# Kernel tuning notes

Hardware: AMD Instinct MI355X
Metric: run time of the kernel (lower is better)

Reference implementation:

```python
import jax, jax.numpy as jnp
import numpy as np

N_NODES = 50000
N_EDGES = 600000
N_GRAPHS = 256
D = 128
D_OUT = 32
NEG_SLOPE = 0.01
EPS = 1e-12


def setup_inputs() -> dict:
    key = jax.random.key(0)
    ks = jax.random.split(key, 10)
    x = jax.random.normal(ks[0], (N_NODES, D), dtype=jnp.float32)
    edge_index = jax.random.randint(ks[1], (2, N_EDGES), 0, N_NODES, dtype=jnp.int64)
    batch = jnp.sort(jax.random.randint(ks[2], (N_NODES,), 0, N_GRAPHS, dtype=jnp.int64))
    s = 1.0 / np.sqrt(D)
    return {
        "x": x,
        "edge_index": edge_index,
        "batch": batch,
        "W_fc1": jax.random.normal(ks[3], (D, D), dtype=jnp.float32) * s,
        "b_fc1": jnp.zeros((D,), dtype=jnp.float32),
        "W_gc1": jax.random.normal(ks[4], (D, D), dtype=jnp.float32) * s,
        "b_gc1": jnp.zeros((D,), dtype=jnp.float32),
        "W_gc2": jax.random.normal(ks[5], (D, D), dtype=jnp.float32) * s,
        "b_gc2": jnp.zeros((D,), dtype=jnp.float32),
        "W_fc2": jax.random.normal(ks[6], (D, D), dtype=jnp.float32) * s,
        "b_fc2": jnp.zeros((D,), dtype=jnp.float32),
        "W_fc3": jax.random.normal(ks[7], (D, D_OUT), dtype=jnp.float32) * s,
        "b_fc3": jnp.zeros((D_OUT,), dtype=jnp.float32),
    }


def _gcn_conv(h, src, dst, inv_sqrt_deg, inv_deg, W, b, n_nodes):
    # GCNConv with self-loops: out = D^{-1/2} (A+I) D^{-1/2} (h @ W) + b
    ht = h @ W  # [N, D]
    coef = inv_sqrt_deg[src] * inv_sqrt_deg[dst]  # [E]
    agg = jax.ops.segment_sum(ht[src] * coef[:, None], dst, num_segments=n_nodes)
    agg = agg + ht * inv_deg[:, None]  # self-loop term
    return agg + b


def reference(x, edge_index, batch, W_fc1, b_fc1, W_gc1, b_gc1, W_gc2, b_gc2,
              W_fc2, b_fc2, W_fc3, b_fc3):
    n = x.shape[0]
    src, dst = edge_index[0], edge_index[1]
    # degree with self-loops (in-degree over targets, unit edge weights)
    deg = jax.ops.segment_sum(jnp.ones_like(dst, dtype=x.dtype), dst, num_segments=n) + 1.0
    inv_sqrt_deg = jax.lax.rsqrt(deg)
    inv_deg = 1.0 / deg

    hx = x @ W_fc1 + b_fc1
    hx = jax.nn.leaky_relu(_gcn_conv(hx, src, dst, inv_sqrt_deg, inv_deg, W_gc1, b_gc1, n), NEG_SLOPE)
    hx = jax.nn.leaky_relu(_gcn_conv(hx, src, dst, inv_sqrt_deg, inv_deg, W_gc2, b_gc2, n), NEG_SLOPE)

    # global mean pool over graphs
    sums = jax.ops.segment_sum(hx, batch, num_segments=N_GRAPHS)  # [G, D]
    counts = jax.ops.segment_sum(jnp.ones((n,), dtype=x.dtype), batch, num_segments=N_GRAPHS)
    pooled = sums / jnp.maximum(counts, 1.0)[:, None]

    # L2 normalize (torch.nn.functional.normalize, p=2, dim=1)
    norm = jnp.sqrt(jnp.sum(pooled * pooled, axis=1, keepdims=True))
    hg = pooled / jnp.maximum(norm, EPS)

    h = jax.nn.leaky_relu(hg @ W_fc2 + b_fc2, NEG_SLOPE)
    out = h @ W_fc3 + b_fc3  # [G, D_OUT]
    return out
```

## Files before the change

kernel.cpp:

```cpp
#include <hip/hip_runtime.h>

#define N_NODES  50000
#define N_EDGES  600000
#define N_GRAPHS 256
#define DOUT     32
#define NEG      0.01f
#define SLOTS    64

typedef __attribute__((ext_vector_type(8))) short short8;
typedef __attribute__((ext_vector_type(4))) float f32x4;

__device__ __forceinline__ unsigned short bf16_rne(float x) {
    unsigned int u = __float_as_uint(x);
    return (unsigned short)((u + 0x7FFFu + ((u >> 16) & 1u)) >> 16);
}


__global__ __launch_bounds__(256) void k_pre(const float* __restrict__ W1,
                                             const float* __restrict__ b1,
                                             const float* __restrict__ W2,
                                             float* __restrict__ W12,
                                             float* __restrict__ b12,
                                             int* __restrict__ counts,
                                             const int* __restrict__ batch,
                                             int* __restrict__ gs,
                                             int* __restrict__ ge) {
    int bid = blockIdx.x;
    int tid = threadIdx.x;
    if (bid < 65) {
        int i = bid * 2 + (tid >> 7);
        int j = tid & 127;
        if (i < 129) {
            const float* left = (i < 128) ? (W1 + i * 128) : b1;
            float acc = 0.f;
#pragma unroll 4
            for (int k = 0; k < 128; ++k) acc += left[k] * W2[k * 128 + j];
            if (i < 128) W12[i * 128 + j] = acc;
            else b12[j] = acc;
        }
    } else if (bid < 261) {
        int i = (bid - 65) * 256 + tid;
        if (i < N_NODES) counts[i] = 0;
    } else {
        int i = (bid - 261) * 256 + tid;
        if (i < N_NODES) {
            int b = batch[i];
            if (i == 0 || batch[i - 1] != b) gs[b] = i;
            if (i == N_NODES - 1 || batch[i + 1] != b) ge[b] = i + 1;
        }
    }
}


__global__ __launch_bounds__(256) void k_degfill(const int* __restrict__ src,
                                                 const int* __restrict__ dst,
                                                 int* __restrict__ counts,
                                                 int* __restrict__ csrs) {
    int e = blockIdx.x * 256 + threadIdx.x;
    if (e < N_EDGES) {
        int s = src[e], d = dst[e];
        int slot = atomicAdd(&counts[d], 1);
        if (slot < SLOTS) csrs[(d << 6) + slot] = s;
    }
}


__global__ __launch_bounds__(256) void k_isd_gemm(
    const int* __restrict__ counts, float* __restrict__ isd,
    const float* __restrict__ Xf, const float* __restrict__ Wsrc,
    const float* __restrict__ bias, unsigned short* __restrict__ Y, int n)
{
    __shared__ short Wl[16384];
    int tid = threadIdx.x;
    int bid = blockIdx.x;
    if (bid < 196) {
        int i = bid * 256 + tid;
        if (i < N_NODES) isd[i] = rsqrtf((float)counts[i] + 1.0f);
        return;
    }
    bid -= 196;

    for (int idx = tid; idx < 16384; idx += 256) {
        float w = Wsrc[idx];
        int k = idx >> 7, c = idx & 127;
        int kt = k >> 5, nt = c >> 4;
        int lane = ((k & 31) >> 3) * 16 + (c & 15);
        int e = k & 7;
        Wl[((kt * 8 + nt) * 64 + lane) * 8 + e] = (short)bf16_rne(w);
    }
    __syncthreads();

    int wid = tid >> 6;
    int lane = tid & 63;
    int r0 = bid * 128 + wid * 32;
    int a0 = r0 + (lane & 15);      if (a0 >= n) a0 = n - 1;
    int a1 = r0 + 16 + (lane & 15); if (a1 >= n) a1 = n - 1;
    int ko = (lane >> 4) * 8;

    f32x4 acc0[8], acc1[8];
    f32x4 zero = {0.f, 0.f, 0.f, 0.f};
#pragma unroll
    for (int t = 0; t < 8; ++t) { acc0[t] = zero; acc1[t] = zero; }

#pragma unroll
    for (int kt = 0; kt < 4; ++kt) {
        int k0 = kt * 32 + ko;
        const float* p0 = Xf + (size_t)a0 * 128 + k0;
        const float* p1 = Xf + (size_t)a1 * 128 + k0;
        float4 u0 = *(const float4*)p0, u1 = *(const float4*)(p0 + 4);
        float4 v0 = *(const float4*)p1, v1 = *(const float4*)(p1 + 4);
        float us[8] = {u0.x, u0.y, u0.z, u0.w, u1.x, u1.y, u1.z, u1.w};
        float vs[8] = {v0.x, v0.y, v0.z, v0.w, v1.x, v1.y, v1.z, v1.w};
        short8 af0, af1;
#pragma unroll
        for (int i = 0; i < 8; ++i) {
            af0[i] = (short)bf16_rne(us[i]);
            af1[i] = (short)bf16_rne(vs[i]);
        }
#pragma unroll
        for (int t = 0; t < 8; ++t) {
            short8 bh = *(const short8*)&Wl[((kt * 8 + t) * 64 + lane) * 8];
            acc0[t] = __builtin_amdgcn_mfma_f32_16x16x32_bf16(af0, bh, acc0[t], 0, 0, 0);
            acc1[t] = __builtin_amdgcn_mfma_f32_16x16x32_bf16(af1, bh, acc1[t], 0, 0, 0);
        }
    }

    int rbase = r0 + (lane >> 4) * 4;
    int col0 = lane & 15;
#pragma unroll
    for (int t = 0; t < 8; ++t) {
        int col = t * 16 + col0;
        float badd = bias[col];
#pragma unroll
        for (int r = 0; r < 4; ++r) {
            int row0 = rbase + r;
            int row1 = rbase + 16 + r;
            if (row0 < n) Y[(size_t)row0 * 128 + col] = bf16_rne(acc0[t][r] + badd);
            if (row1 < n) Y[(size_t)row1 * 128 + col] = bf16_rne(acc1[t][r] + badd);
        }
    }
}


__global__ __launch_bounds__(256) void k_gemm_mfma(
    const unsigned short* __restrict__ Xh, const float* __restrict__ Wsrc,
    unsigned short* __restrict__ Y, int n)
{
    __shared__ short Wl[16384];
    int tid = threadIdx.x;
    for (int idx = tid; idx < 16384; idx += 256) {
        float w = Wsrc[idx];
        int k = idx >> 7, c = idx & 127;
        int kt = k >> 5, nt = c >> 4;
        int lane = ((k & 31) >> 3) * 16 + (c & 15);
        int e = k & 7;
        Wl[((kt * 8 + nt) * 64 + lane) * 8 + e] = (short)bf16_rne(w);
    }
    __syncthreads();

    int wid = tid >> 6;
    int lane = tid & 63;
    int r0 = blockIdx.x * 128 + wid * 32;
    int a0 = r0 + (lane & 15);      if (a0 >= n) a0 = n - 1;
    int a1 = r0 + 16 + (lane & 15); if (a1 >= n) a1 = n - 1;
    int ko = (lane >> 4) * 8;

    f32x4 acc0[8], acc1[8];
    f32x4 zero = {0.f, 0.f, 0.f, 0.f};
#pragma unroll
    for (int t = 0; t < 8; ++t) { acc0[t] = zero; acc1[t] = zero; }

#pragma unroll
    for (int kt = 0; kt < 4; ++kt) {
        int k0 = kt * 32 + ko;
        short8 af0 = *(const short8*)(Xh + (size_t)a0 * 128 + k0);
        short8 af1 = *(const short8*)(Xh + (size_t)a1 * 128 + k0);
#pragma unroll
        for (int t = 0; t < 8; ++t) {
            short8 bh = *(const short8*)&Wl[((kt * 8 + t) * 64 + lane) * 8];
            acc0[t] = __builtin_amdgcn_mfma_f32_16x16x32_bf16(af0, bh, acc0[t], 0, 0, 0);
            acc1[t] = __builtin_amdgcn_mfma_f32_16x16x32_bf16(af1, bh, acc1[t], 0, 0, 0);
        }
    }

    int rbase = r0 + (lane >> 4) * 4;
    int col0 = lane & 15;
#pragma unroll
    for (int t = 0; t < 8; ++t) {
        int col = t * 16 + col0;
#pragma unroll
        for (int r = 0; r < 4; ++r) {
            int row0 = rbase + r;
            int row1 = rbase + 16 + r;
            if (row0 < n) Y[(size_t)row0 * 128 + col] = bf16_rne(acc0[t][r]);
            if (row1 < n) Y[(size_t)row1 * 128 + col] = bf16_rne(acc1[t][r]);
        }
    }
}


__global__ __launch_bounds__(256) void k_agg(const unsigned short* __restrict__ HT,
                                             const int* __restrict__ csrs,
                                             const int* __restrict__ counts,
                                             const float* __restrict__ isd,
                                             const float* __restrict__ bias,
                                             unsigned short* __restrict__ OUT, int n) {
    int node = blockIdx.x * 4 + (threadIdx.x >> 6);
    int lane = threadIdx.x & 63;
    if (node >= n) return;
    const unsigned int* H = (const unsigned int*)HT;
    int base = node << 6;
    int cnt = counts[node]; cnt = cnt < SLOTS ? cnt : SLOTS;

    float is = isd[node];
    unsigned int su = H[(size_t)node * 64 + lane];
    float2 b = ((const float2*)bias)[lane];

    float acc0 = 0.f, acc1 = 0.f, acc2 = 0.f, acc3 = 0.f;
    int j = 0;
    for (; j + 8 <= cnt; j += 8) {
        int sx[8];
#pragma unroll
        for (int q = 0; q < 8; ++q) sx[q] = csrs[base + j + q];
        float cf[8];
#pragma unroll
        for (int q = 0; q < 8; ++q) cf[q] = isd[sx[q]];
        unsigned int v[8];
#pragma unroll
        for (int q = 0; q < 8; ++q) v[q] = H[(size_t)sx[q] * 64 + lane];
#pragma unroll
        for (int q = 0; q < 8; ++q) {
            float c = cf[q] * is;
            float f0 = __uint_as_float(v[q] << 16);
            float f1 = __uint_as_float(v[q] & 0xFFFF0000u);
            if (q & 1) { acc2 += f0 * c; acc3 += f1 * c; }
            else       { acc0 += f0 * c; acc1 += f1 * c; }
        }
    }
    for (; j + 4 <= cnt; j += 4) {
        int sx[4];
#pragma unroll
        for (int q = 0; q < 4; ++q) sx[q] = csrs[base + j + q];
        float cf[4];
#pragma unroll
        for (int q = 0; q < 4; ++q) cf[q] = isd[sx[q]];
        unsigned int v[4];
#pragma unroll
        for (int q = 0; q < 4; ++q) v[q] = H[(size_t)sx[q] * 64 + lane];
#pragma unroll
        for (int q = 0; q < 4; ++q) {
            float c = cf[q] * is;
            float f0 = __uint_as_float(v[q] << 16);
            float f1 = __uint_as_float(v[q] & 0xFFFF0000u);
            if (q & 1) { acc2 += f0 * c; acc3 += f1 * c; }
            else       { acc0 += f0 * c; acc1 += f1 * c; }
        }
    }
    for (; j < cnt; ++j) {
        int s = csrs[base + j];
        float c = isd[s] * is;
        unsigned int v = H[(size_t)s * 64 + lane];
        acc0 += __uint_as_float(v << 16) * c;
        acc1 += __uint_as_float(v & 0xFFFF0000u) * c;
    }

    float invd = is * is;
    float sv0 = __uint_as_float(su << 16);
    float sv1 = __uint_as_float(su & 0xFFFF0000u);
    float ox = acc0 + acc2 + sv0 * invd + b.x;
    float oy = acc1 + acc3 + sv1 * invd + b.y;
    ox = ox > 0.f ? ox : ox * NEG;
    oy = oy > 0.f ? oy : oy * NEG;
    unsigned int pk = (unsigned int)bf16_rne(ox) | ((unsigned int)bf16_rne(oy) << 16);
    ((unsigned int*)OUT)[(size_t)node * 64 + lane] = pk;
}


__global__ __launch_bounds__(256) void k_pool_final(const unsigned short* __restrict__ Hn,
                                                    const int* __restrict__ gs,
                                                    const int* __restrict__ ge,
                                                    const float* __restrict__ W2,
                                                    const float* __restrict__ b2,
                                                    const float* __restrict__ W3,
                                                    const float* __restrict__ b3,
                                                    float* __restrict__ out) {
    __shared__ float part[4][128];
    __shared__ float red[128];
    __shared__ float h1[128];
    int g = blockIdx.x, tid = threadIdx.x;
    int c2 = tid & 63, rr = tid >> 6;
    int s = gs[g], e = ge[g];
    const unsigned int* H = (const unsigned int*)Hn;
    float2 acc = make_float2(0.f, 0.f);
    for (int r = s + rr; r < e; r += 4) {
        unsigned int v = H[(size_t)r * 64 + c2];
        acc.x += __uint_as_float(v << 16);
        acc.y += __uint_as_float(v & 0xFFFF0000u);
    }
    part[rr][c2 * 2] = acc.x;
    part[rr][c2 * 2 + 1] = acc.y;
    __syncthreads();
    float mean = 0.f;
    if (tid < 128) {
        mean = (part[0][tid] + part[1][tid] + part[2][tid] + part[3][tid])
               / fmaxf((float)(e - s), 1.f);
        red[tid] = mean * mean;
    }
    __syncthreads();
    for (int off = 64; off > 0; off >>= 1) {
        if (tid < off) red[tid] += red[tid + off];
        __syncthreads();
    }
    if (tid < 128) {
        float norm = sqrtf(red[0]);
        part[0][tid] = mean / fmaxf(norm, 1e-12f);
    }
    __syncthreads();
    if (tid < 128) {
        float a = b2[tid];
#pragma unroll 8
        for (int k = 0; k < 128; ++k) a += part[0][k] * W2[k * 128 + tid];
        a = a > 0.f ? a : a * NEG;
        h1[tid] = a;
    }
    __syncthreads();
    if (tid < DOUT) {
        float a2 = b3[tid];
#pragma unroll 8
        for (int k = 0; k < 128; ++k) a2 += h1[k] * W3[k * DOUT + tid];
        out[g * DOUT + tid] = a2;
    }
}


extern "C" void kernel_launch(void* const* d_in, const int* in_sizes, int n_in,
                              void* d_out, int out_size, void* d_ws, size_t ws_size,
                              hipStream_t stream) {
    const float* x      = (const float*)d_in[0];
    const int*   ei     = (const int*)d_in[1];
    const int*   batch  = (const int*)d_in[2];
    const float* W_fc1  = (const float*)d_in[3];
    const float* b_fc1  = (const float*)d_in[4];
    const float* W_gc1  = (const float*)d_in[5];
    const float* b_gc1  = (const float*)d_in[6];
    const float* W_gc2  = (const float*)d_in[7];
    const float* b_gc2  = (const float*)d_in[8];
    const float* W_fc2  = (const float*)d_in[9];
    const float* b_fc2  = (const float*)d_in[10];
    const float* W_fc3  = (const float*)d_in[11];
    const float* b_fc3  = (const float*)d_in[12];
    float* out = (float*)d_out;

    const int N = N_NODES, E = N_EDGES;
    const int* e_src = ei;
    const int* e_dst = ei + E;

    char* ws = (char*)d_ws;
    unsigned short* H0     = (unsigned short*)(ws + 0);
    unsigned short* H1     = (unsigned short*)(ws + 12800000);
    float*          isd    = (float*)(ws + 25600000);
    int*            csrs   = (int*)  (ws + 25800000);
    int*            counts = (int*)  (ws + 38600000);
    int*            gs     = (int*)  (ws + 38800000);
    int*            ge     = (int*)  (ws + 38801024);
    float*          W12    = (float*)(ws + 38802048);
    float*          b12    = (float*)(ws + 38867584);

    const int EB = (E + 255) / 256;
    const int GB = (N + 127) / 128;

    k_pre<<<457, 256, 0, stream>>>(W_fc1, b_fc1, W_gc1, W12, b12, counts, batch, gs, ge);
    k_degfill<<<EB, 256, 0, stream>>>(e_src, e_dst, counts, csrs);
    k_isd_gemm<<<196 + GB, 256, 0, stream>>>(counts, isd, x, W12, b12, H1, N);
    k_agg<<<(N + 3) / 4, 256, 0, stream>>>(H1, csrs, counts, isd, b_gc1, H0, N);
    k_gemm_mfma<<<GB, 256, 0, stream>>>(H0, W_gc2, H1, N);
    k_agg<<<(N + 3) / 4, 256, 0, stream>>>(H1, csrs, counts, isd, b_gc2, H0, N);
    k_pool_final<<<N_GRAPHS, 256, 0, stream>>>(H0, gs, ge, W_fc2, b_fc2, W_fc3, b_fc3, out);

    (void)in_sizes; (void)n_in; (void)out_size; (void)ws_size;
}
```

Before: 162.0 us.

## Fuse edge fill into first GEMM and split CSR into primary/overflow slots

The degree/CSR fill is merged into the first GEMM launch as extra blocks, so both run concurrently and one launch is removed. The separate inverse-sqrt-degree array is dropped and recomputed with rsqrtf from the counts inside the aggregation kernel. Neighbor lists move to a compact 16-slot primary array plus a 48-slot overflow array, which shrinks the footprint the aggregation reads for typical degrees. In exchange, the fill blocks compete with the GEMM blocks for the GPU, and aggregation does an extra rsqrt per edge and takes a less unrolled path for high-degree nodes.

```diff
diff --git a/kernel.cpp b/kernel.cpp
--- a/kernel.cpp
+++ b/kernel.cpp
@@ -6,6 +6,9 @@
 #define DOUT     32
 #define NEG      0.01f
 #define SLOTS    64
+#define PSLOTS   16
+#define OSLOTS   48
+#define GB_GEMM  391
 
 typedef __attribute__((ext_vector_type(8))) short short8;
 typedef __attribute__((ext_vector_type(4))) float f32x4;
@@ -52,33 +55,26 @@
 }
 
 
-__global__ __launch_bounds__(256) void k_degfill(const int* __restrict__ src,
-                                                 const int* __restrict__ dst,
-                                                 int* __restrict__ counts,
-                                                 int* __restrict__ csrs) {
-    int e = blockIdx.x * 256 + threadIdx.x;
-    if (e < N_EDGES) {
-        int s = src[e], d = dst[e];
-        int slot = atomicAdd(&counts[d], 1);
-        if (slot < SLOTS) csrs[(d << 6) + slot] = s;
-    }
-}
-
-
-__global__ __launch_bounds__(256) void k_isd_gemm(
-    const int* __restrict__ counts, float* __restrict__ isd,
+__global__ __launch_bounds__(256) void k_fill_gemm(
+    const int* __restrict__ src, const int* __restrict__ dst,
+    int* __restrict__ counts, int* __restrict__ csrp, int* __restrict__ csro,
     const float* __restrict__ Xf, const float* __restrict__ Wsrc,
     const float* __restrict__ bias, unsigned short* __restrict__ Y, int n)
 {
     __shared__ short Wl[16384];
+    int bid = blockIdx.x;
     int tid = threadIdx.x;
-    int bid = blockIdx.x;
-    if (bid < 196) {
-        int i = bid * 256 + tid;
-        if (i < N_NODES) isd[i] = rsqrtf((float)counts[i] + 1.0f);
+
+    if (bid >= GB_GEMM) {
+        int e = (bid - GB_GEMM) * 256 + tid;
+        if (e < N_EDGES) {
+            int s = src[e], d = dst[e];
+            int slot = atomicAdd(&counts[d], 1);
+            if (slot < PSLOTS) csrp[(d << 4) + slot] = s;
+            else if (slot < SLOTS) csro[d * OSLOTS + slot - PSLOTS] = s;
+        }
         return;
     }
-    bid -= 196;
 
     for (int idx = tid; idx < 16384; idx += 256) {
         float w = Wsrc[idx];
@@ -200,65 +196,74 @@
 
 
 __global__ __launch_bounds__(256) void k_agg(const unsigned short* __restrict__ HT,
-                                             const int* __restrict__ csrs,
+                                             const int* __restrict__ csrp,
+                                             const int* __restrict__ csro,
                                              const int* __restrict__ counts,
-                                             const float* __restrict__ isd,
                                              const float* __restrict__ bias,
                                              unsigned short* __restrict__ OUT, int n) {
     int node = blockIdx.x * 4 + (threadIdx.x >> 6);
     int lane = threadIdx.x & 63;
     if (node >= n) return;
     const unsigned int* H = (const unsigned int*)HT;
-    int base = node << 6;
-    int cnt = counts[node]; cnt = cnt < SLOTS ? cnt : SLOTS;
-
-    float is = isd[node];
+    int deg = counts[node];
+    float is = rsqrtf((float)deg + 1.0f);
+    int c1 = deg < PSLOTS ? deg : PSLOTS;
+    int base = node << 4;
+
     unsigned int su = H[(size_t)node * 64 + lane];
     float2 b = ((const float2*)bias)[lane];
 
     float acc0 = 0.f, acc1 = 0.f, acc2 = 0.f, acc3 = 0.f;
     int j = 0;
-    for (; j + 8 <= cnt; j += 8) {
+    for (; j + 8 <= c1; j += 8) {
         int sx[8];
 #pragma unroll
-        for (int q = 0; q < 8; ++q) sx[q] = csrs[base + j + q];
-        float cf[8];
-#pragma unroll
-        for (int q = 0; q < 8; ++q) cf[q] = isd[sx[q]];
+        for (int q = 0; q < 8; ++q) sx[q] = csrp[base + j + q];
+        int dg[8];
+#pragma unroll
+        for (int q = 0; q < 8; ++q) dg[q] = counts[sx[q]];
         unsigned int v[8];
 #pragma unroll
         for (int q = 0; q < 8; ++q) v[q] = H[(size_t)sx[q] * 64 + lane];
 #pragma unroll
         for (int q = 0; q < 8; ++q) {
-            float c = cf[q] * is;
+            float c = rsqrtf((float)dg[q] + 1.0f) * is;
             float f0 = __uint_as_float(v[q] << 16);
             float f1 = __uint_as_float(v[q] & 0xFFFF0000u);
             if (q & 1) { acc2 += f0 * c; acc3 += f1 * c; }
             else       { acc0 += f0 * c; acc1 += f1 * c; }
         }
     }
-    for (; j + 4 <= cnt; j += 4) {
+    for (; j + 4 <= c1; j += 4) {
         int sx[4];
 #pragma unroll
-        for (int q = 0; q < 4; ++q) sx[q] = csrs[base + j + q];
-        float cf[4];
-#pragma unroll
-        for (int q = 0; q < 4; ++q) cf[q] = isd[sx[q]];
+        for (int q = 0; q < 4; ++q) sx[q] = csrp[base + j + q];
+        int dg[4];
+#pragma unroll
+        for (int q = 0; q < 4; ++q) dg[q] = counts[sx[q]];
         unsigned int v[4];
 #pragma unroll
         for (int q = 0; q < 4; ++q) v[q] = H[(size_t)sx[q] * 64 + lane];
 #pragma unroll
         for (int q = 0; q < 4; ++q) {
-            float c = cf[q] * is;
+            float c = rsqrtf((float)dg[q] + 1.0f) * is;
             float f0 = __uint_as_float(v[q] << 16);
             float f1 = __uint_as_float(v[q] & 0xFFFF0000u);
             if (q & 1) { acc2 += f0 * c; acc3 += f1 * c; }
             else       { acc0 += f0 * c; acc1 += f1 * c; }
         }
     }
-    for (; j < cnt; ++j) {
-        int s = csrs[base + j];
-        float c = isd[s] * is;
+    for (; j < c1; ++j) {
+        int s = csrp[base + j];
+        float c = rsqrtf((float)counts[s] + 1.0f) * is;
+        unsigned int v = H[(size_t)s * 64 + lane];
+        acc0 += __uint_as_float(v << 16) * c;
+        acc1 += __uint_as_float(v & 0xFFFF0000u) * c;
+    }
+    int c2 = deg < SLOTS ? deg : SLOTS;
+    for (j = PSLOTS; j < c2; ++j) {
+        int s = csro[node * OSLOTS + j - PSLOTS];
+        float c = rsqrtf((float)counts[s] + 1.0f) * is;
         unsigned int v = H[(size_t)s * 64 + lane];
         acc0 += __uint_as_float(v << 16) * c;
         acc1 += __uint_as_float(v & 0xFFFF0000u) * c;
@@ -358,23 +363,22 @@
     char* ws = (char*)d_ws;
     unsigned short* H0     = (unsigned short*)(ws + 0);
     unsigned short* H1     = (unsigned short*)(ws + 12800000);
-    float*          isd    = (float*)(ws + 25600000);
-    int*            csrs   = (int*)  (ws + 25800000);
-    int*            counts = (int*)  (ws + 38600000);
-    int*            gs     = (int*)  (ws + 38800000);
-    int*            ge     = (int*)  (ws + 38801024);
-    float*          W12    = (float*)(ws + 38802048);
-    float*          b12    = (float*)(ws + 38867584);
+    int*            csrp   = (int*)  (ws + 25600000);
+    int*            csro   = (int*)  (ws + 28800000);
+    int*            counts = (int*)  (ws + 38400000);
+    int*            gs     = (int*)  (ws + 38600000);
+    int*            ge     = (int*)  (ws + 38601024);
+    float*          W12    = (float*)(ws + 38602048);
+    float*          b12    = (float*)(ws + 38667584);
 
     const int EB = (E + 255) / 256;
-    const int GB = (N + 127) / 128;
 
     k_pre<<<457, 256, 0, stream>>>(W_fc1, b_fc1, W_gc1, W12, b12, counts, batch, gs, ge);
-    k_degfill<<<EB, 256, 0, stream>>>(e_src, e_dst, counts, csrs);
-    k_isd_gemm<<<196 + GB, 256, 0, stream>>>(counts, isd, x, W12, b12, H1, N);
-    k_agg<<<(N + 3) / 4, 256, 0, stream>>>(H1, csrs, counts, isd, b_gc1, H0, N);
-    k_gemm_mfma<<<GB, 256, 0, stream>>>(H0, W_gc2, H1, N);
-    k_agg<<<(N + 3) / 4, 256, 0, stream>>>(H1, csrs, counts, isd, b_gc2, H0, N);
+    k_fill_gemm<<<GB_GEMM + EB, 256, 0, stream>>>(e_src, e_dst, counts, csrp, csro,
+                                                  x, W12, b12, H1, N);
+    k_agg<<<(N + 3) / 4, 256, 0, stream>>>(H1, csrp, csro, counts, b_gc1, H0, N);
+    k_gemm_mfma<<<GB_GEMM, 256, 0, stream>>>(H0, W_gc2, H1, N);
+    k_agg<<<(N + 3) / 4, 256, 0, stream>>>(H1, csrp, csro, counts, b_gc2, H0, N);
     k_pool_final<<<N_GRAPHS, 256, 0, stream>>>(H0, gs, ge, W_fc2, b_fc2, W_fc3, b_fc3, out);
 
     (void)in_sizes; (void)n_in; (void)out_size; (void)ws_size;
```

Result: faster. 157.1 us, median of 2 (-3.0%).
